# Performance work log

Hardware: AMD Instinct MI355X
Metric: run time of the kernel (lower is better)

## Reference

```python
import jax, jax.numpy as jnp
import numpy as np

H, D = 12, 768
DH = D // H  # 64

def setup_inputs() -> dict:
    key = jax.random.key(0)
    ks = jax.random.split(key, 9)
    s = 0.02
    x  = jax.random.normal(ks[0], (8, 1024, D), dtype=jnp.float32)
    Wq = jax.random.normal(ks[1], (H, D, DH), dtype=jnp.float32) * s
    Wk = jax.random.normal(ks[2], (H, D, DH), dtype=jnp.float32) * s
    Wv = jax.random.normal(ks[3], (H, D, DH), dtype=jnp.float32) * s
    bq = jax.random.normal(ks[4], (H, DH), dtype=jnp.float32) * s
    bk = jax.random.normal(ks[5], (H, DH), dtype=jnp.float32) * s
    bv = jax.random.normal(ks[6], (H, DH), dtype=jnp.float32) * s
    Wo = jax.random.normal(ks[7], (D, D), dtype=jnp.float32) * s
    bo = jax.random.normal(ks[8], (D,), dtype=jnp.float32) * s
    return {"x": x, "Wq": Wq, "Wk": Wk, "Wv": Wv, "bq": bq, "bk": bk, "bv": bv, "Wo": Wo, "bo": bo}

def reference(x, Wq, Wk, Wv, bq, bk, bv, Wo, bo):
    # x: [B,S,D]; per-head projections batched over heads: [B,H,S,DH]
    q = jnp.einsum('bsd,hde->bhse', x, Wq) + bq[None, :, None, :]
    k = jnp.einsum('bsd,hde->bhse', x, Wk) + bk[None, :, None, :]
    v = jnp.einsum('bsd,hde->bhse', x, Wv) + bv[None, :, None, :]
    scores = jnp.einsum('bhse,bhte->bhst', q, k) / jnp.sqrt(jnp.float32(DH))
    probs = jax.nn.softmax(scores, axis=-1)  # dropout is identity (p=0 / eval)
    ctx = jnp.einsum('bhst,bhte->bhse', probs, v)  # [B,H,S,DH]
    B, _, S, _ = ctx.shape
    # concat heads along feature dim (head order matches torch cat order)
    ctx = jnp.transpose(ctx, (0, 2, 1, 3)).reshape(B, S, H * DH)
    out = jnp.einsum('bsd,de->bse', ctx, Wo) + bo
    return out
```

## Files before the change

### kernel.cpp

```cpp
#include <hip/hip_runtime.h>
#include <math.h>


constexpr int NB  = 8;
constexpr int SEQ = 1024;
constexpr int NH  = 12;
constexpr int DM  = 768;
constexpr int DHD = 64;
constexpr int MROWS = NB * SEQ;
constexpr int NQKV  = 3 * NH * DHD;

typedef __attribute__((ext_vector_type(8))) short short8;
typedef __attribute__((ext_vector_type(4))) float f32x4;

#define MFMA16(a,b,c) __builtin_amdgcn_mfma_f32_16x16x32_bf16((a),(b),(c),0,0,0)

#if __has_builtin(__builtin_amdgcn_exp2f)
#define EXP2(x) __builtin_amdgcn_exp2f(x)
#else
#define EXP2(x) exp2f(x)
#endif

__device__ __forceinline__ unsigned short f2bf(float f) {
    unsigned u = __float_as_uint(f);
    return (unsigned short)((u + 0x7fffu + ((u >> 16) & 1u)) >> 16);
}
__device__ __forceinline__ unsigned short f2bf_fast(float f) {
    return (unsigned short)((__float_as_uint(f) + 0x8000u) >> 16);
}

__device__ __forceinline__ void gl_lds16(const unsigned short* g, unsigned short* l) {
    __builtin_amdgcn_global_load_lds(
        (const __attribute__((address_space(1))) void*)g,
        (__attribute__((address_space(3))) void*)l, 16, 0, 0);
}

__device__ __forceinline__ void stageA(unsigned short* lds, const unsigned short* gbase,
                                       int i, int ln, int ldg) {
    int r    = i * 16 + (ln >> 2);
    int cpos = ln & 3;
    int cdat = (cpos - (r >> 1)) & 3;
    gl_lds16(gbase + (size_t)r * ldg + cdat * 8, lds + i * 512);
}
__device__ __forceinline__ short8 ldA(const unsigned short* buf, int row, int quad) {
    int c = (quad + (row >> 1)) & 3;
    return *(const short8*)&buf[row * 32 + c * 8];
}

__device__ __forceinline__ void stageK(unsigned short* lds, const unsigned short* gbase,
                                       int i, int ln, int ldg) {
    int r    = i * 8 + (ln >> 3);
    int cpos = ln & 7;
    int cdat = (cpos - r) & 7;
    gl_lds16(gbase + (size_t)r * ldg + cdat * 8, lds + i * 512);
}
__device__ __forceinline__ short8 ldK(const unsigned short* buf, int row, int chunk) {
    int c = (chunk + row) & 7;
    return *(const short8*)&buf[row * 64 + c * 8];
}

__global__ __launch_bounds__(256) void prep_k(
    const float* __restrict__ x,
    const float* __restrict__ Wq, const float* __restrict__ Wk,
    const float* __restrict__ Wv, const float* __restrict__ Wo,
    unsigned short* __restrict__ xb, unsigned short* __restrict__ wt,
    unsigned short* __restrict__ wot) {
    __shared__ float tb[64][65];
    const int blk = blockIdx.x, tid = threadIdx.x;
    if (blk < 6144) {
        const int i = blk * 256 + tid;
        float4 v = ((const float4*)x)[i];
        ushort4 o;
        o.x = f2bf(v.x); o.y = f2bf(v.y); o.z = f2bf(v.z); o.w = f2bf(v.w);
        ((ushort4*)xb)[i] = o;
        return;
    }
    const int t = blk - 6144;
    const int job = t / 144, lb = t % 144;
    const float* W;
    unsigned short* dst;
    int C, r0, c0;
    if (job < 3) {
        const float* Ws = (job == 0) ? Wq : (job == 1 ? Wk : Wv);
        const int h = lb / 12, rb = lb % 12;
        W = Ws + (size_t)h * (DM * DHD);
        dst = wt + (size_t)(job * 12 + h) * (DM * DHD);
        C = DHD; r0 = rb * 64; c0 = 0;
    } else {
        W = Wo; dst = wot; C = DM;
        r0 = (lb / 12) * 64; c0 = (lb % 12) * 64;
    }
    const int rr = tid >> 2, cc = (tid & 3) * 16;
#pragma unroll
    for (int j = 0; j < 16; j += 4) {
        float4 v = *(const float4*)&W[(size_t)(r0 + rr) * C + c0 + cc + j];
        tb[rr][cc + j + 0] = v.x;
        tb[rr][cc + j + 1] = v.y;
        tb[rr][cc + j + 2] = v.z;
        tb[rr][cc + j + 3] = v.w;
    }
    __syncthreads();
#pragma unroll
    for (int j = 0; j < 16; ++j)
        dst[(size_t)(c0 + rr) * DM + r0 + cc + j] = f2bf(tb[cc + j][rr]);
}

__global__ __launch_bounds__(256, 3) void qkv_mfma_k(
    const unsigned short* __restrict__ xb, const unsigned short* __restrict__ wt,
    const float* __restrict__ bq, const float* __restrict__ bk, const float* __restrict__ bv,
    unsigned short* __restrict__ qb, unsigned short* __restrict__ kb,
    unsigned short* __restrict__ vT) {
    __shared__ unsigned short Ah[128 * 32], Bh[128 * 32];

    const int tid = threadIdx.x;
    const int wv = tid >> 6, ln = tid & 63, quad = ln >> 4, lnid = ln & 15;
    const int wvm = wv >> 1, wvn = wv & 1;
    const int row0 = blockIdx.x * 128, col0 = blockIdx.y * 128;

    f32x4 acc[4][4];
#pragma unroll
    for (int i = 0; i < 4; ++i)
#pragma unroll
        for (int j = 0; j < 4; ++j) acc[i][j] = (f32x4){0.f, 0.f, 0.f, 0.f};

    const unsigned short* Ahg = xb + (size_t)row0 * DM;
    const unsigned short* Bhg = wt + (size_t)col0 * DM;

    for (int kc = 0; kc < DM; kc += 32) {
        __syncthreads();
        stageA(Ah, Ahg + kc, wv * 2, ln, DM);
        stageA(Ah, Ahg + kc, wv * 2 + 1, ln, DM);
        stageA(Bh, Bhg + kc, wv * 2, ln, DM);
        stageA(Bh, Bhg + kc, wv * 2 + 1, ln, DM);
        __syncthreads();

        short8 a[4], b[4];
#pragma unroll
        for (int i = 0; i < 4; ++i) a[i] = ldA(Ah, wvm * 64 + i * 16 + lnid, quad);
#pragma unroll
        for (int j = 0; j < 4; ++j) b[j] = ldA(Bh, wvn * 64 + j * 16 + lnid, quad);
#pragma unroll
        for (int i = 0; i < 4; ++i)
#pragma unroll
            for (int j = 0; j < 4; ++j) acc[i][j] = MFMA16(a[i], b[j], acc[i][j]);
    }

    const int sel = (col0 >= 2 * DM) ? 2 : (col0 >= DM ? 1 : 0);
    const float scale = (sel == 0) ? 0.18033688011112042f : 1.0f;
    const float* bias = (sel == 0) ? bq : (sel == 1 ? bk : bv);
    unsigned short* oh = (sel == 0) ? qb : kb;

#pragma unroll
    for (int i = 0; i < 4; ++i) {
#pragma unroll
        for (int j = 0; j < 4; ++j) {
            const int col = col0 + wvn * 64 + j * 16 + lnid;
            const int he = col - sel * DM;
            const int hh2 = he >> 6, ee = he & 63;
            const float bs = bias[he];
            if (sel < 2) {
#pragma unroll
                for (int r = 0; r < 4; ++r) {
                    const int srow = row0 + wvm * 64 + i * 16 + quad * 4 + r;
                    const int bb = srow >> 10, ss = srow & (SEQ - 1);
                    oh[((size_t)(bb * NH + hh2) * SEQ + ss) * DHD + ee] =
                        f2bf((acc[i][j][r] + bs) * scale);
                }
            } else {
                const int srow = row0 + wvm * 64 + i * 16 + quad * 4;
                const int bb = srow >> 10, ss = srow & (SEQ - 1);
                ushort4 pk;
                pk.x = f2bf(acc[i][j][0] + bs);
                pk.y = f2bf(acc[i][j][1] + bs);
                pk.z = f2bf(acc[i][j][2] + bs);
                pk.w = f2bf(acc[i][j][3] + bs);
                *(ushort4*)&vT[((size_t)(bb * NH + hh2) * DHD + ee) * SEQ + ss] = pk;
            }
        }
    }
}

__global__ __launch_bounds__(256, 3) void attn_mfma_k(
    const unsigned short* __restrict__ qb, const unsigned short* __restrict__ kb,
    const unsigned short* __restrict__ vT, unsigned short* __restrict__ ctb) {
    __shared__ unsigned short ksh[2][64 * 64], vsm[2][64 * 64];
    __shared__ unsigned short ps[128 * 72];

    const int tid = threadIdx.x;
    const int wv = tid >> 6, ln = tid & 63, quad = ln >> 4, lnid = ln & 15;
    const int bhid = blockIdx.x % 96, qt = blockIdx.x / 96;
    const int b = bhid / NH, h = bhid % NH;
    const int q0 = qt * 128;
    const unsigned short* qhb = qb + (size_t)bhid * (SEQ * DHD);
    const unsigned short* khb = kb + (size_t)bhid * (SEQ * DHD);
    const unsigned short* vTb = vT + (size_t)bhid * (DHD * SEQ);

    short8 qf[2][2];
#pragma unroll
    for (int mt = 0; mt < 2; ++mt) {
        const int srow = q0 + wv * 32 + mt * 16 + lnid;
#pragma unroll
        for (int ks_ = 0; ks_ < 2; ++ks_)
            qf[mt][ks_] = *(const short8*)(qhb + (size_t)srow * DHD + ks_ * 32 + quad * 8);
    }

    f32x4 ctx[2][4];
#pragma unroll
    for (int i = 0; i < 2; ++i)
#pragma unroll
        for (int j = 0; j < 4; ++j) ctx[i][j] = (f32x4){0.f, 0.f, 0.f, 0.f};
    float lsum[2][4] = {};

    stageK(ksh[0], khb, wv * 2, ln, DHD);
    stageK(ksh[0], khb, wv * 2 + 1, ln, DHD);
    stageK(vsm[0], vTb, wv * 2, ln, SEQ);
    stageK(vsm[0], vTb, wv * 2 + 1, ln, SEQ);

    for (int kt = 0; kt < SEQ / 64; ++kt) {
        const int cur = kt & 1;
        __syncthreads();
        if (kt + 1 < SEQ / 64) {
            const unsigned short* kn = khb + (kt + 1) * 64 * DHD;
            const unsigned short* vn = vTb + (kt + 1) * 64;
            stageK(ksh[cur ^ 1], kn, wv * 2, ln, DHD);
            stageK(ksh[cur ^ 1], kn, wv * 2 + 1, ln, DHD);
            stageK(vsm[cur ^ 1], vn, wv * 2, ln, SEQ);
            stageK(vsm[cur ^ 1], vn, wv * 2 + 1, ln, SEQ);
        }

        f32x4 sc[2][4];
#pragma unroll
        for (int i = 0; i < 2; ++i)
#pragma unroll
            for (int j = 0; j < 4; ++j) sc[i][j] = (f32x4){0.f, 0.f, 0.f, 0.f};
#pragma unroll
        for (int ks_ = 0; ks_ < 2; ++ks_) {
#pragma unroll
            for (int nt = 0; nt < 4; ++nt) {
                short8 k_h = ldK(ksh[cur], nt * 16 + lnid, ks_ * 4 + quad);
                sc[0][nt] = MFMA16(qf[0][ks_], k_h, sc[0][nt]);
                sc[1][nt] = MFMA16(qf[1][ks_], k_h, sc[1][nt]);
            }
        }

#pragma unroll
        for (int mt = 0; mt < 2; ++mt)
#pragma unroll
            for (int nt = 0; nt < 4; ++nt)
#pragma unroll
                for (int r = 0; r < 4; ++r) {
                    float p = EXP2(sc[mt][nt][r]);
                    lsum[mt][r] += p;
                    ps[(wv * 32 + mt * 16 + quad * 4 + r) * 72 + nt * 16 + lnid] =
                        f2bf_fast(p);
                }

#pragma unroll
        for (int kvs = 0; kvs < 2; ++kvs) {
            short8 pa0 = *(const short8*)&ps[(wv * 32 + lnid) * 72 + kvs * 32 + quad * 8];
            short8 pa1 = *(const short8*)&ps[(wv * 32 + 16 + lnid) * 72 + kvs * 32 + quad * 8];
#pragma unroll
            for (int nt = 0; nt < 4; ++nt) {
                short8 v8 = ldK(vsm[cur], nt * 16 + lnid, kvs * 4 + quad);
                ctx[0][nt] = MFMA16(pa0, v8, ctx[0][nt]);
                ctx[1][nt] = MFMA16(pa1, v8, ctx[1][nt]);
            }
        }
    }

#pragma unroll
    for (int mt = 0; mt < 2; ++mt) {
#pragma unroll
        for (int r = 0; r < 4; ++r) {
            float s = lsum[mt][r];
#pragma unroll
            for (int off = 1; off < 16; off <<= 1) s += __shfl_xor(s, off, 64);
            const float inv = 1.0f / s;
            const int srow = b * SEQ + q0 + wv * 32 + mt * 16 + quad * 4 + r;
#pragma unroll
            for (int nt = 0; nt < 4; ++nt)
                ctb[(size_t)srow * DM + h * DHD + nt * 16 + lnid] =
                    f2bf(ctx[mt][nt][r] * inv);
        }
    }
}

__global__ __launch_bounds__(256, 3) void out_mfma_k(
    const unsigned short* __restrict__ ctb, const unsigned short* __restrict__ wot,
    const float* __restrict__ bo, float* __restrict__ out) {
    __shared__ unsigned short Ah[128 * 32], Bh[128 * 32];

    const int tid = threadIdx.x;
    const int wv = tid >> 6, ln = tid & 63, quad = ln >> 4, lnid = ln & 15;
    const int wvm = wv >> 1, wvn = wv & 1;
    const int row0 = blockIdx.x * 128, col0 = blockIdx.y * 128;

    f32x4 acc[4][4];
#pragma unroll
    for (int i = 0; i < 4; ++i)
#pragma unroll
        for (int j = 0; j < 4; ++j) acc[i][j] = (f32x4){0.f, 0.f, 0.f, 0.f};

    const unsigned short* Ahg = ctb + (size_t)row0 * DM;
    const unsigned short* Bhg = wot + (size_t)col0 * DM;

    for (int kc = 0; kc < DM; kc += 32) {
        __syncthreads();
        stageA(Ah, Ahg + kc, wv * 2, ln, DM);
        stageA(Ah, Ahg + kc, wv * 2 + 1, ln, DM);
        stageA(Bh, Bhg + kc, wv * 2, ln, DM);
        stageA(Bh, Bhg + kc, wv * 2 + 1, ln, DM);
        __syncthreads();

        short8 a[4], b[4];
#pragma unroll
        for (int i = 0; i < 4; ++i) a[i] = ldA(Ah, wvm * 64 + i * 16 + lnid, quad);
#pragma unroll
        for (int j = 0; j < 4; ++j) b[j] = ldA(Bh, wvn * 64 + j * 16 + lnid, quad);
#pragma unroll
        for (int i = 0; i < 4; ++i)
#pragma unroll
            for (int j = 0; j < 4; ++j) acc[i][j] = MFMA16(a[i], b[j], acc[i][j]);
    }

#pragma unroll
    for (int i = 0; i < 4; ++i)
#pragma unroll
        for (int j = 0; j < 4; ++j) {
            const int col = col0 + wvn * 64 + j * 16 + lnid;
            const float bs = bo[col];
#pragma unroll
            for (int r = 0; r < 4; ++r) {
                const int srow = row0 + wvm * 64 + i * 16 + quad * 4 + r;
                out[(size_t)srow * DM + col] = acc[i][j][r] + bs;
            }
        }
}

extern "C" void kernel_launch(void* const* d_in, const int* in_sizes, int n_in,
                              void* d_out, int out_size, void* d_ws, size_t ws_size,
                              hipStream_t stream) {
    const float* x  = (const float*)d_in[0];
    const float* Wq = (const float*)d_in[1];
    const float* Wk = (const float*)d_in[2];
    const float* Wv = (const float*)d_in[3];
    const float* bq = (const float*)d_in[4];
    const float* bk = (const float*)d_in[5];
    const float* bv = (const float*)d_in[6];
    const float* Wo = (const float*)d_in[7];
    const float* bo = (const float*)d_in[8];
    float* out = (float*)d_out;

    char* w = (char*)d_ws;
    const size_t elsX = (size_t)MROWS * DM;
    const size_t elsQ = (size_t)NB * NH * SEQ * DHD;
    unsigned short* xb  = (unsigned short*)w;
    unsigned short* ctb = xb;
    size_t off = elsX * 2;
    unsigned short* wt  = (unsigned short*)(w + off); off += (size_t)NQKV * DM * 2;
    unsigned short* wot = (unsigned short*)(w + off); off += (size_t)DM * DM * 2;
    unsigned short* qbp = (unsigned short*)(w + off); off += elsQ * 2;
    unsigned short* kbp = (unsigned short*)(w + off); off += elsQ * 2;
    unsigned short* vTp = (unsigned short*)(w + off); off += elsQ * 2;

    prep_k<<<dim3(6144 + 576), 256, 0, stream>>>(x, Wq, Wk, Wv, Wo, xb, wt, wot);
    qkv_mfma_k<<<dim3(MROWS / 128, NQKV / 128), 256, 0, stream>>>(
        xb, wt, bq, bk, bv, qbp, kbp, vTp);
    attn_mfma_k<<<dim3(768), 256, 0, stream>>>(qbp, kbp, vTp, ctb);
    out_mfma_k<<<dim3(MROWS / 128, DM / 128), 256, 0, stream>>>(ctb, wot, bo, out);
}
```

Measured before the change: 203.5 us.

## Double-buffer LDS staging in projection GEMMs and shrink output GEMM tile

Both the QKV and output projection GEMMs now use two LDS buffers, so the next K-slice is staged while MFMAs run on the current one, and one barrier per iteration is removed. The output GEMM tile is cut from 128x128 to 128x64, which doubles its grid to about 768 blocks and improves CU occupancy on the 256-CU device. The costs are more LDS per block and lower per-block reuse of the activation tile in the output GEMM.

```diff
diff --git a/kernel.cpp b/kernel.cpp
--- a/kernel.cpp
+++ b/kernel.cpp
@@ -110,7 +110,7 @@
     const float* __restrict__ bq, const float* __restrict__ bk, const float* __restrict__ bv,
     unsigned short* __restrict__ qb, unsigned short* __restrict__ kb,
     unsigned short* __restrict__ vT) {
-    __shared__ unsigned short Ah[128 * 32], Bh[128 * 32];
+    __shared__ unsigned short Ah[2][128 * 32], Bh[2][128 * 32];
 
     const int tid = threadIdx.x;
     const int wv = tid >> 6, ln = tid & 63, quad = ln >> 4, lnid = ln & 15;
@@ -126,19 +126,28 @@
     const unsigned short* Ahg = xb + (size_t)row0 * DM;
     const unsigned short* Bhg = wt + (size_t)col0 * DM;
 
-    for (int kc = 0; kc < DM; kc += 32) {
+    stageA(Ah[0], Ahg, wv * 2, ln, DM);
+    stageA(Ah[0], Ahg, wv * 2 + 1, ln, DM);
+    stageA(Bh[0], Bhg, wv * 2, ln, DM);
+    stageA(Bh[0], Bhg, wv * 2 + 1, ln, DM);
+
+    constexpr int NIT = DM / 32;
+    for (int it = 0; it < NIT; ++it) {
+        const int cur = it & 1;
         __syncthreads();
-        stageA(Ah, Ahg + kc, wv * 2, ln, DM);
-        stageA(Ah, Ahg + kc, wv * 2 + 1, ln, DM);
-        stageA(Bh, Bhg + kc, wv * 2, ln, DM);
-        stageA(Bh, Bhg + kc, wv * 2 + 1, ln, DM);
-        __syncthreads();
+        if (it + 1 < NIT) {
+            const int kc = (it + 1) * 32;
+            stageA(Ah[cur ^ 1], Ahg + kc, wv * 2, ln, DM);
+            stageA(Ah[cur ^ 1], Ahg + kc, wv * 2 + 1, ln, DM);
+            stageA(Bh[cur ^ 1], Bhg + kc, wv * 2, ln, DM);
+            stageA(Bh[cur ^ 1], Bhg + kc, wv * 2 + 1, ln, DM);
+        }
 
         short8 a[4], b[4];
 #pragma unroll
-        for (int i = 0; i < 4; ++i) a[i] = ldA(Ah, wvm * 64 + i * 16 + lnid, quad);
-#pragma unroll
-        for (int j = 0; j < 4; ++j) b[j] = ldA(Bh, wvn * 64 + j * 16 + lnid, quad);
+        for (int i = 0; i < 4; ++i) a[i] = ldA(Ah[cur], wvm * 64 + i * 16 + lnid, quad);
+#pragma unroll
+        for (int j = 0; j < 4; ++j) b[j] = ldA(Bh[cur], wvn * 64 + j * 16 + lnid, quad);
 #pragma unroll
         for (int i = 0; i < 4; ++i)
 #pragma unroll
@@ -288,46 +297,53 @@
 __global__ __launch_bounds__(256, 3) void out_mfma_k(
     const unsigned short* __restrict__ ctb, const unsigned short* __restrict__ wot,
     const float* __restrict__ bo, float* __restrict__ out) {
-    __shared__ unsigned short Ah[128 * 32], Bh[128 * 32];
+    __shared__ unsigned short Ah[2][128 * 32], Bh[2][64 * 32];
 
     const int tid = threadIdx.x;
     const int wv = tid >> 6, ln = tid & 63, quad = ln >> 4, lnid = ln & 15;
     const int wvm = wv >> 1, wvn = wv & 1;
-    const int row0 = blockIdx.x * 128, col0 = blockIdx.y * 128;
-
-    f32x4 acc[4][4];
+    const int row0 = blockIdx.x * 128, col0 = blockIdx.y * 64;
+
+    f32x4 acc[4][2];
 #pragma unroll
     for (int i = 0; i < 4; ++i)
 #pragma unroll
-        for (int j = 0; j < 4; ++j) acc[i][j] = (f32x4){0.f, 0.f, 0.f, 0.f};
+        for (int j = 0; j < 2; ++j) acc[i][j] = (f32x4){0.f, 0.f, 0.f, 0.f};
 
     const unsigned short* Ahg = ctb + (size_t)row0 * DM;
     const unsigned short* Bhg = wot + (size_t)col0 * DM;
 
-    for (int kc = 0; kc < DM; kc += 32) {
+    stageA(Ah[0], Ahg, wv * 2, ln, DM);
+    stageA(Ah[0], Ahg, wv * 2 + 1, ln, DM);
+    stageA(Bh[0], Bhg, wv, ln, DM);
+
+    constexpr int NIT = DM / 32;
+    for (int it = 0; it < NIT; ++it) {
+        const int cur = it & 1;
         __syncthreads();
-        stageA(Ah, Ahg + kc, wv * 2, ln, DM);
-        stageA(Ah, Ahg + kc, wv * 2 + 1, ln, DM);
-        stageA(Bh, Bhg + kc, wv * 2, ln, DM);
-        stageA(Bh, Bhg + kc, wv * 2 + 1, ln, DM);
-        __syncthreads();
-
-        short8 a[4], b[4];
-#pragma unroll
-        for (int i = 0; i < 4; ++i) a[i] = ldA(Ah, wvm * 64 + i * 16 + lnid, quad);
-#pragma unroll
-        for (int j = 0; j < 4; ++j) b[j] = ldA(Bh, wvn * 64 + j * 16 + lnid, quad);
+        if (it + 1 < NIT) {
+            const int kc = (it + 1) * 32;
+            stageA(Ah[cur ^ 1], Ahg + kc, wv * 2, ln, DM);
+            stageA(Ah[cur ^ 1], Ahg + kc, wv * 2 + 1, ln, DM);
+            stageA(Bh[cur ^ 1], Bhg + kc, wv, ln, DM);
+        }
+
+        short8 a[4], b[2];
+#pragma unroll
+        for (int i = 0; i < 4; ++i) a[i] = ldA(Ah[cur], wvm * 64 + i * 16 + lnid, quad);
+#pragma unroll
+        for (int j = 0; j < 2; ++j) b[j] = ldA(Bh[cur], wvn * 32 + j * 16 + lnid, quad);
 #pragma unroll
         for (int i = 0; i < 4; ++i)
 #pragma unroll
-            for (int j = 0; j < 4; ++j) acc[i][j] = MFMA16(a[i], b[j], acc[i][j]);
+            for (int j = 0; j < 2; ++j) acc[i][j] = MFMA16(a[i], b[j], acc[i][j]);
     }
 
 #pragma unroll
     for (int i = 0; i < 4; ++i)
 #pragma unroll
-        for (int j = 0; j < 4; ++j) {
-            const int col = col0 + wvn * 64 + j * 16 + lnid;
+        for (int j = 0; j < 2; ++j) {
+            const int col = col0 + wvn * 32 + j * 16 + lnid;
             const float bs = bo[col];
 #pragma unroll
             for (int r = 0; r < 4; ++r) {
@@ -367,5 +383,5 @@
     qkv_mfma_k<<<dim3(MROWS / 128, NQKV / 128), 256, 0, stream>>>(
         xb, wt, bq, bk, bv, qbp, kbp, vTp);
     attn_mfma_k<<<dim3(768), 256, 0, stream>>>(qbp, kbp, vTp, ctb);
-    out_mfma_k<<<dim3(MROWS / 128, DM / 128), 256, 0, stream>>>(ctb, wot, bo, out);
-}
+    out_mfma_k<<<dim3(MROWS / 128, DM / 64), 256, 0, stream>>>(ctb, wot, bo, out);
+}
```

Measured after the change: 203.5 us. Within noise of the previous version (-0.0%).
